# Kernel tuning notes

Measured on AMD Instinct MI355X. Metric: run time of the kernel, lower is better.

## Reference

```python
import jax, jax.numpy as jnp
import numpy as np
from jax import lax

B, C, O, H, W = 4, 96, 96, 128, 128
K = 3      # kernel size everywhere
D = 2      # dilation of dconv
KK = K * K


def conv2d(x, w, b, pad, dil=1):
    # x: [B,C,H,W], w: [O,C,K,K]
    y = lax.conv_general_dilated(
        x, w, window_strides=(1, 1), padding=[(pad, pad), (pad, pad)],
        rhs_dilation=(dil, dil), dimension_numbers=('NCHW', 'OIHW', 'NCHW'))
    return y + b[None, :, None, None]


def bilinear_sample(img, py, px):
    # img: [B,C,H,W]; py,px: [B,KK,H,W] float sample coords (zero outside)
    y0 = jnp.floor(py)
    x0 = jnp.floor(px)
    wy = py - y0
    wx = px - x0
    flat = img.reshape(B, 1, C, H * W)  # broadcast over KK

    def gather(yi, xi):
        valid = (yi >= 0) & (yi < H) & (xi >= 0) & (xi < W)
        yc = jnp.clip(yi, 0, H - 1).astype(jnp.int32)
        xc = jnp.clip(xi, 0, W - 1).astype(jnp.int32)
        idx = (yc * W + xc).reshape(B, KK, 1, H * W)
        g = jnp.take_along_axis(flat, idx, axis=3)  # [B,KK,C,H*W]
        g = g.reshape(B, KK, C, H, W)
        return g * valid.reshape(B, KK, 1, H, W)

    v00 = gather(y0, x0)
    v01 = gather(y0, x0 + 1)
    v10 = gather(y0 + 1, x0)
    v11 = gather(y0 + 1, x0 + 1)
    wy = wy[:, :, None]
    wx = wx[:, :, None]
    return ((1 - wy) * ((1 - wx) * v00 + wx * v01)
            + wy * ((1 - wx) * v10 + wx * v11))


def setup_inputs() -> dict:
    key = jax.random.key(0)
    ks = jax.random.split(key, 7)
    x = jax.random.normal(ks[0], (B, C, H, W), jnp.float32)
    s = 1.0 / np.sqrt(C * K * K)  # torch default conv init bound
    u = lambda k, shape: jax.random.uniform(k, shape, jnp.float32, -s, s)
    return dict(
        x=x,
        dconv_w=u(ks[1], (O, C, K, K)), dconv_b=u(ks[2], (O,)),
        off_w=u(ks[3], (2 * KK, C, K, K)), off_b=u(ks[4], (2 * KK,)),
        def_w=u(ks[5], (O, C, K, K)), def_b=u(ks[6], (O,)),
    )


def reference(x, dconv_w, dconv_b, off_w, off_b, def_w, def_b):
    # dilated conv + relu + residual (self.conv is unused in the original forward)
    x1 = conv2d(x, dconv_w, dconv_b, pad=D, dil=D)
    x3 = x + jax.nn.relu(x1)

    # offset prediction: [B, 2*KK, H, W] -> (dy, dx) per kernel tap
    offset = conv2d(x3, off_w, off_b, pad=1)
    off = offset.reshape(B, KK, 2, H, W)
    dy, dx = off[:, :, 0], off[:, :, 1]

    # base sampling grid: output pixel + kernel tap - padding
    ki, kj = jnp.meshgrid(jnp.arange(K), jnp.arange(K), indexing='ij')
    ky = (ki.reshape(-1) - (K - 1) // 2).astype(jnp.float32)  # [KK]
    kx = (kj.reshape(-1) - (K - 1) // 2).astype(jnp.float32)
    ygrid = jnp.arange(H, dtype=jnp.float32)[:, None]
    xgrid = jnp.arange(W, dtype=jnp.float32)[None, :]
    py = ygrid[None, None] + ky[None, :, None, None] + dy  # [B,KK,H,W]
    px = xgrid[None, None] + kx[None, :, None, None] + dx

    sampled = bilinear_sample(x3, py, px)  # [B,KK,C,H,W]
    out = jnp.einsum('bkchw,ock->bohw', sampled, def_w.reshape(O, C, KK))
    return out + def_b[None, :, None, None]
```

## Files before the change

### kernel.cpp

```cpp
#include <hip/hip_runtime.h>
#include <hip/hip_bf16.h>

#define BD 4
#define CD 96
#define OD 96
#define HD 128
#define WD 128
#define HWD (HD*WD)

typedef __attribute__((ext_vector_type(8))) short bfrag;
typedef __attribute__((ext_vector_type(4))) float ffrag;

__device__ __forceinline__ short f2bs(float f) {
    __hip_bfloat16 h = __float2bfloat16(f);
    return *reinterpret_cast<short*>(&h);
}

__device__ __forceinline__ int swizzle1024(int gid) {
    return ((gid & 7) << 7) | (gid >> 3);
}

__global__ __launch_bounds__(256) void k_transpose(const float* __restrict__ x,
                                                   short* __restrict__ xb16) {
    __shared__ short tile[128 * 104];
    int pix0 = blockIdx.x * 128;
    int b = pix0 / HWD; int hw0 = pix0 % HWD;
    int tid = threadIdx.x;

    for (int e = tid; e < 96*32; e += 256) {
        int c = e >> 5, g = e & 31;
        float4 v = *(const float4*)(x + ((size_t)(b*96 + c))*HWD + hw0 + 4*g);
        tile[(4*g+0)*104 + c] = f2bs(v.x);
        tile[(4*g+1)*104 + c] = f2bs(v.y);
        tile[(4*g+2)*104 + c] = f2bs(v.z);
        tile[(4*g+3)*104 + c] = f2bs(v.w);
    }
    __syncthreads();
    for (int e = tid; e < 128*12; e += 256) {
        int px = e / 12, c8 = e % 12;
        bfrag v = *(const bfrag*)(tile + px*104 + c8*8);
        *(bfrag*)(xb16 + ((size_t)(pix0 + px))*96 + c8*8) = v;
    }
}

__global__ void k_repack(const float* __restrict__ dconv_w,
                         const float* __restrict__ off_w,
                         const float* __restrict__ def_w,
                         short* __restrict__ wB1,
                         short* __restrict__ wB2,
                         short* __restrict__ wB) {
    int t = blockIdx.x * blockDim.x + threadIdx.x;
    if (t < 27648) {
        int j = t & 7; int l = (t >> 3) & 63; int tile = t >> 9;
        int s = tile >> 1, nt = tile & 1;
        int k = 32*s + (l >> 4)*8 + j;
        int o = 16*nt + (l & 15);
        int c = k % 96, tap = k / 96;
        wB2[t] = (o < 18) ? f2bs(off_w[(o*96 + c)*9 + tap]) : (short)0;
    }
    if (t < 82944) {
        int j = t & 7; int l = (t >> 3) & 63; int tile = t >> 9;
        int s = tile / 6, nt = tile % 6;
        int k = 32*s + (l >> 4)*8 + j;
        int o = 16*nt + (l & 15);
        int c = k % 96, tap = k / 96;
        wB1[t] = f2bs(dconv_w[(o*96 + c)*9 + tap]);
        wB[t]  = f2bs(def_w [(o*96 + c)*9 + tap]);
    }
}

__global__ __launch_bounds__(256, 4) void k_conv1(const float* __restrict__ x,
                                                  const short* __restrict__ xb16,
                                                  const short* __restrict__ wB,
                                                  const float* __restrict__ bias,
                                                  short* __restrict__ x3b) {
    int pix0 = swizzle1024(blockIdx.x) * 64;
    int b = pix0 / HWD; int hw0 = pix0 % HWD;
    int h = hw0 / WD; int w0 = hw0 % WD;
    int tid = threadIdx.x;
    int l = tid & 63, wv = tid >> 6;
    int q = l >> 4, mr = l & 15;
    int wbase = w0 + 16*wv;
    const short* xb = xb16 + ((size_t)b * HWD) * 96;
    const bfrag az = {0,0,0,0,0,0,0,0};

    ffrag acc[6];
    #pragma unroll
    for (int nt = 0; nt < 6; nt++) acc[nt] = ffrag{0.f,0.f,0.f,0.f};

    #pragma unroll 1
    for (int tap = 0; tap < 9; tap++) {
        int y = h + (tap/3)*2 - 2;
        if ((unsigned)y >= HD) continue;
        int xx = wbase + mr + (tap%3)*2 - 2;
        int xxc = min(max(xx, 0), WD-1);
        bool vx = (unsigned)xx < WD;
        const short* abase = xb + ((size_t)(y*WD + xxc))*96 + q*8;
        #pragma unroll
        for (int sc = 0; sc < 3; sc++) {
            const short* wb = wB + ((size_t)((tap*3+sc)*6)*64 + l)*8;
            bfrag a = *(const bfrag*)(abase + sc*32);
            if (!vx) a = az;
            #pragma unroll
            for (int nt = 0; nt < 6; nt++) {
                bfrag bb = *(const bfrag*)(wb + nt*512);
                acc[nt] = __builtin_amdgcn_mfma_f32_16x16x32_bf16(a, bb, acc[nt], 0, 0, 0);
            }
        }
    }

    int hwb = hw0 + 16*wv + q*4;
    #pragma unroll
    for (int nt = 0; nt < 6; nt++) {
        int o = 16*nt + mr;
        float bo = bias[o];
        float4 xr = *(const float4*)(x + ((size_t)(b*96 + o))*HWD + hwb);
        short* op = x3b + ((size_t)(b*HWD + hwb))*96 + o;
        op[0]   = f2bs(xr.x + fmaxf(acc[nt][0] + bo, 0.f));
        op[96]  = f2bs(xr.y + fmaxf(acc[nt][1] + bo, 0.f));
        op[192] = f2bs(xr.z + fmaxf(acc[nt][2] + bo, 0.f));
        op[288] = f2bs(xr.w + fmaxf(acc[nt][3] + bo, 0.f));
    }
}

__global__ __launch_bounds__(256, 4) void k_deform(const short* __restrict__ x3b,
                                                   const short* __restrict__ wB2,
                                                   const float* __restrict__ off_b,
                                                   const short* __restrict__ wB,
                                                   const float* __restrict__ def_b,
                                                   float* __restrict__ out) {
    __shared__ float offsb[64][20];

    int pix0 = swizzle1024(blockIdx.x) * 64;
    int b = pix0 / HWD; int hw0 = pix0 % HWD;
    int h = hw0 / WD; int w0 = hw0 % WD;
    int tid = threadIdx.x;
    int l = tid & 63, wv = tid >> 6;
    int q = l >> 4, mr = l & 15;
    int wbase = w0 + 16*wv;
    const short* xb = x3b + ((size_t)b * HWD) * 96;
    const bfrag az = {0,0,0,0,0,0,0,0};

    ffrag oa[2];
    oa[0] = ffrag{0.f,0.f,0.f,0.f};
    oa[1] = ffrag{0.f,0.f,0.f,0.f};

    #pragma unroll 1
    for (int tap = 0; tap < 9; tap++) {
        int y = h + tap/3 - 1;
        if ((unsigned)y >= HD) continue;
        int xx = wbase + mr + tap%3 - 1;
        int xxc = min(max(xx, 0), WD-1);
        bool vx = (unsigned)xx < WD;
        const short* abase = xb + ((size_t)(y*WD + xxc))*96 + q*8;
        #pragma unroll
        for (int sc = 0; sc < 3; sc++) {
            const short* wb = wB2 + ((size_t)((tap*3+sc)*2)*64 + l)*8;
            bfrag b0 = *(const bfrag*)(wb);
            bfrag b1 = *(const bfrag*)(wb + 512);
            bfrag a = *(const bfrag*)(abase + sc*32);
            if (!vx) a = az;
            oa[0] = __builtin_amdgcn_mfma_f32_16x16x32_bf16(a, b0, oa[0], 0, 0, 0);
            oa[1] = __builtin_amdgcn_mfma_f32_16x16x32_bf16(a, b1, oa[1], 0, 0, 0);
        }
    }
    {
        int row = 16*wv + q*4;
        float bo0 = off_b[mr];
        #pragma unroll
        for (int r = 0; r < 4; r++) offsb[row + r][mr] = oa[0][r] + bo0;
        if (mr < 2) {
            float bo1 = off_b[16 + mr];
            #pragma unroll
            for (int r = 0; r < 4; r++) offsb[row + r][16 + mr] = oa[1][r] + bo1;
        }
    }

    ffrag acc[6];
    #pragma unroll
    for (int nt = 0; nt < 6; nt++) acc[nt] = ffrag{0.f,0.f,0.f,0.f};

    #pragma unroll 1
    for (int tap = 0; tap < 9; tap++) {
        const short* pp[4];
        float fb[4];
        {
            int lp = 16*wv + mr;
            int w = wbase + mr;
            float dy = offsb[lp][2*tap];
            float dx = offsb[lp][2*tap + 1];
            float py  = (float)(h + tap/3 - 1) + dy;
            float pxf = (float)(w + tap%3 - 1) + dx;
            float y0f = floorf(py), x0f = floorf(pxf);
            float wy = py - y0f, wx = pxf - x0f;
            int y0 = (int)y0f, x0 = (int)x0f;
            int y1 = y0 + 1, x1 = x0 + 1;
            bool vy0 = (unsigned)y0 < HD, vy1 = (unsigned)y1 < HD;
            bool vx0 = (unsigned)x0 < WD, vx1 = (unsigned)x1 < WD;
            fb[0] = (vy0 && vx0) ? (1.f-wy)*(1.f-wx) : 0.f;
            fb[1] = (vy0 && vx1) ? (1.f-wy)*wx       : 0.f;
            fb[2] = (vy1 && vx0) ? wy*(1.f-wx)       : 0.f;
            fb[3] = (vy1 && vx1) ? wy*wx             : 0.f;
            int yc0 = min(max(y0,0),HD-1), yc1 = min(max(y1,0),HD-1);
            int xc0 = min(max(x0,0),WD-1), xc1 = min(max(x1,0),WD-1);
            pp[0] = xb + ((size_t)(yc0*WD + xc0))*96 + q*8;
            pp[1] = xb + ((size_t)(yc0*WD + xc1))*96 + q*8;
            pp[2] = xb + ((size_t)(yc1*WD + xc0))*96 + q*8;
            pp[3] = xb + ((size_t)(yc1*WD + xc1))*96 + q*8;
        }
        #pragma unroll
        for (int sc = 0; sc < 3; sc++) {
            int s = tap*3 + sc;
            const short* wb = wB + ((size_t)(s*6)*64 + l)*8;
            bfrag bbf[6];
            #pragma unroll
            for (int nt = 0; nt < 6; nt++) bbf[nt] = *(const bfrag*)(wb + nt*512);
            bfrag c00 = *(const bfrag*)(pp[0] + sc*32);
            bfrag c01 = *(const bfrag*)(pp[1] + sc*32);
            bfrag c10 = *(const bfrag*)(pp[2] + sc*32);
            bfrag c11 = *(const bfrag*)(pp[3] + sc*32);
            const int* i00 = (const int*)&c00;
            const int* i01 = (const int*)&c01;
            const int* i10 = (const int*)&c10;
            const int* i11 = (const int*)&c11;
            float f00 = fb[0], f01 = fb[1];
            float f10 = fb[2], f11 = fb[3];
            int ap[4];
            #pragma unroll
            for (int d = 0; d < 4; d++) {
                float a0 = __int_as_float(((unsigned)i00[d]) << 16);
                float b0f = __int_as_float(((unsigned)i01[d]) << 16);
                float c0f = __int_as_float(((unsigned)i10[d]) << 16);
                float d0 = __int_as_float(((unsigned)i11[d]) << 16);
                float a1 = __int_as_float(i00[d] & 0xffff0000);
                float b1f = __int_as_float(i01[d] & 0xffff0000);
                float c1f = __int_as_float(i10[d] & 0xffff0000);
                float d1 = __int_as_float(i11[d] & 0xffff0000);
                float rlo = f00*a0 + f01*b0f + f10*c0f + f11*d0;
                float rhi = f00*a1 + f01*b1f + f10*c1f + f11*d1;
                ap[d] = (int)((unsigned short)f2bs(rlo)) |
                        ((int)((unsigned short)f2bs(rhi)) << 16);
            }
            bfrag a = *(const bfrag*)ap;
            #pragma unroll
            for (int nt = 0; nt < 6; nt++)
                acc[nt] = __builtin_amdgcn_mfma_f32_16x16x32_bf16(a, bbf[nt], acc[nt], 0, 0, 0);
        }
    }

    int hwb = hw0 + 16*wv + q*4;
    #pragma unroll
    for (int nt = 0; nt < 6; nt++) {
        int o = 16*nt + mr;
        float bo = def_b[o];
        float4 v;
        v.x = acc[nt][0] + bo; v.y = acc[nt][1] + bo;
        v.z = acc[nt][2] + bo; v.w = acc[nt][3] + bo;
        *(float4*)(out + ((size_t)(b*96 + o))*HWD + hwb) = v;
    }
}

extern "C" void kernel_launch(void* const* d_in, const int* in_sizes, int n_in,
                              void* d_out, int out_size, void* d_ws, size_t ws_size,
                              hipStream_t stream) {
    const float* x       = (const float*)d_in[0];
    const float* dconv_w = (const float*)d_in[1];
    const float* dconv_b = (const float*)d_in[2];
    const float* off_w   = (const float*)d_in[3];
    const float* off_b   = (const float*)d_in[4];
    const float* def_w   = (const float*)d_in[5];
    const float* def_b   = (const float*)d_in[6];
    float* out = (float*)d_out;

    char* ws = (char*)d_ws;
    short* xb16 = (short*)(ws);
    short* x3b  = (short*)(ws + 12582912);
    short* wB1  = (short*)(ws + 25165824);
    short* wB2  = (short*)(ws + 25331712);
    short* wB   = (short*)(ws + 25387008);

    k_repack<<<324, 256, 0, stream>>>(dconv_w, off_w, def_w, wB1, wB2, wB);
    k_transpose<<<(BD*HWD)/128, 256, 0, stream>>>(x, xb16);
    k_conv1<<<(BD*HWD)/64, 256, 0, stream>>>(x, xb16, wB1, dconv_b, x3b);
    k_deform<<<(BD*HWD)/64, 256, 0, stream>>>(x3b, wB2, off_b, wB, def_b, out);
}
```

Baseline: 192.9 us.

## Split output channels across waves and share sampled tiles via LDS

In the conv and deformable kernels, each wave now computes two 16-pixel M tiles against half of the output channels (3 N tiles) instead of one M tile against all 6. This halves the weight fragments each wave loads and reuses each loaded weight across two A tiles. The deform kernel moves to 32-pixel, 128-thread blocks. It stages the bilinear-interpolated A fragments in a double-buffered shared buffer so both waves can use both pixel tiles, at the cost of one barrier per tap. The transpose block size is halved, launch bounds are lowered, and addressing switches to 32-bit byte offsets.

```diff
diff --git a/kernel.cpp b/kernel.cpp
--- a/kernel.cpp
+++ b/kernel.cpp
@@ -19,16 +19,19 @@
 __device__ __forceinline__ int swizzle1024(int gid) {
     return ((gid & 7) << 7) | (gid >> 3);
 }
+__device__ __forceinline__ int swizzle2048(int gid) {
+    return ((gid & 7) << 8) | (gid >> 3);
+}
 
 __global__ __launch_bounds__(256) void k_transpose(const float* __restrict__ x,
                                                    short* __restrict__ xb16) {
-    __shared__ short tile[128 * 104];
-    int pix0 = blockIdx.x * 128;
+    __shared__ short tile[64 * 104];
+    int pix0 = blockIdx.x * 64;
     int b = pix0 / HWD; int hw0 = pix0 % HWD;
     int tid = threadIdx.x;
 
-    for (int e = tid; e < 96*32; e += 256) {
-        int c = e >> 5, g = e & 31;
+    for (int e = tid; e < 96*16; e += 256) {
+        int c = e >> 4, g = e & 15;
         float4 v = *(const float4*)(x + ((size_t)(b*96 + c))*HWD + hw0 + 4*g);
         tile[(4*g+0)*104 + c] = f2bs(v.x);
         tile[(4*g+1)*104 + c] = f2bs(v.y);
@@ -36,7 +39,7 @@
         tile[(4*g+3)*104 + c] = f2bs(v.w);
     }
     __syncthreads();
-    for (int e = tid; e < 128*12; e += 256) {
+    for (int e = tid; e < 64*12; e += 256) {
         int px = e / 12, c8 = e % 12;
         bfrag v = *(const bfrag*)(tile + px*104 + c8*8);
         *(bfrag*)(xb16 + ((size_t)(pix0 + px))*96 + c8*8) = v;
@@ -69,7 +72,7 @@
     }
 }
 
-__global__ __launch_bounds__(256, 4) void k_conv1(const float* __restrict__ x,
+__global__ __launch_bounds__(256, 3) void k_conv1(const float* __restrict__ x,
                                                   const short* __restrict__ xb16,
                                                   const short* __restrict__ wB,
                                                   const float* __restrict__ bias,
@@ -79,66 +82,81 @@
     int h = hw0 / WD; int w0 = hw0 % WD;
     int tid = threadIdx.x;
     int l = tid & 63, wv = tid >> 6;
+    int pr = wv >> 1, tg = wv & 1;
     int q = l >> 4, mr = l & 15;
-    int wbase = w0 + 16*wv;
-    const short* xb = xb16 + ((size_t)b * HWD) * 96;
+    int wq = w0 + 32*pr;
+    const char* xbc = (const char*)(xb16 + ((size_t)b * HWD) * 96);
     const bfrag az = {0,0,0,0,0,0,0,0};
 
-    ffrag acc[6];
+    ffrag acc[2][3];
     #pragma unroll
-    for (int nt = 0; nt < 6; nt++) acc[nt] = ffrag{0.f,0.f,0.f,0.f};
+    for (int mt = 0; mt < 2; mt++)
+        #pragma unroll
+        for (int n = 0; n < 3; n++) acc[mt][n] = ffrag{0.f,0.f,0.f,0.f};
 
     #pragma unroll 1
     for (int tap = 0; tap < 9; tap++) {
         int y = h + (tap/3)*2 - 2;
         if ((unsigned)y >= HD) continue;
-        int xx = wbase + mr + (tap%3)*2 - 2;
-        int xxc = min(max(xx, 0), WD-1);
-        bool vx = (unsigned)xx < WD;
-        const short* abase = xb + ((size_t)(y*WD + xxc))*96 + q*8;
+        unsigned aoff[2]; bool vx[2];
+        #pragma unroll
+        for (int mt = 0; mt < 2; mt++) {
+            int xx = wq + 16*mt + mr + (tap%3)*2 - 2;
+            int xxc = min(max(xx, 0), WD-1);
+            vx[mt] = (unsigned)xx < WD;
+            aoff[mt] = (unsigned)(((y*WD + xxc)*96 + q*8) * 2);
+        }
         #pragma unroll
         for (int sc = 0; sc < 3; sc++) {
-            const short* wb = wB + ((size_t)((tap*3+sc)*6)*64 + l)*8;
-            bfrag a = *(const bfrag*)(abase + sc*32);
-            if (!vx) a = az;
-            #pragma unroll
-            for (int nt = 0; nt < 6; nt++) {
-                bfrag bb = *(const bfrag*)(wb + nt*512);
-                acc[nt] = __builtin_amdgcn_mfma_f32_16x16x32_bf16(a, bb, acc[nt], 0, 0, 0);
+            const short* wb = wB + ((size_t)((tap*3+sc)*6 + 3*tg)*64 + l)*8;
+            bfrag bb[3];
+            #pragma unroll
+            for (int n = 0; n < 3; n++) bb[n] = *(const bfrag*)(wb + n*512);
+            #pragma unroll
+            for (int mt = 0; mt < 2; mt++) {
+                bfrag a = *(const bfrag*)(xbc + aoff[mt] + sc*64);
+                if (!vx[mt]) a = az;
+                #pragma unroll
+                for (int n = 0; n < 3; n++)
+                    acc[mt][n] = __builtin_amdgcn_mfma_f32_16x16x32_bf16(a, bb[n], acc[mt][n], 0, 0, 0);
             }
         }
     }
 
-    int hwb = hw0 + 16*wv + q*4;
     #pragma unroll
-    for (int nt = 0; nt < 6; nt++) {
-        int o = 16*nt + mr;
-        float bo = bias[o];
-        float4 xr = *(const float4*)(x + ((size_t)(b*96 + o))*HWD + hwb);
-        short* op = x3b + ((size_t)(b*HWD + hwb))*96 + o;
-        op[0]   = f2bs(xr.x + fmaxf(acc[nt][0] + bo, 0.f));
-        op[96]  = f2bs(xr.y + fmaxf(acc[nt][1] + bo, 0.f));
-        op[192] = f2bs(xr.z + fmaxf(acc[nt][2] + bo, 0.f));
-        op[288] = f2bs(xr.w + fmaxf(acc[nt][3] + bo, 0.f));
-    }
-}
-
-__global__ __launch_bounds__(256, 4) void k_deform(const short* __restrict__ x3b,
+    for (int mt = 0; mt < 2; mt++) {
+        int hwb = hw0 + 32*pr + 16*mt + q*4;
+        #pragma unroll
+        for (int n = 0; n < 3; n++) {
+            int o = 16*(3*tg + n) + mr;
+            float bo = bias[o];
+            float4 xr = *(const float4*)(x + ((size_t)(b*96 + o))*HWD + hwb);
+            short* op = x3b + ((size_t)(b*HWD + hwb))*96 + o;
+            op[0]   = f2bs(xr.x + fmaxf(acc[mt][n][0] + bo, 0.f));
+            op[96]  = f2bs(xr.y + fmaxf(acc[mt][n][1] + bo, 0.f));
+            op[192] = f2bs(xr.z + fmaxf(acc[mt][n][2] + bo, 0.f));
+            op[288] = f2bs(xr.w + fmaxf(acc[mt][n][3] + bo, 0.f));
+        }
+    }
+}
+
+__global__ __launch_bounds__(128, 3) void k_deform(const short* __restrict__ x3b,
                                                    const short* __restrict__ wB2,
                                                    const float* __restrict__ off_b,
                                                    const short* __restrict__ wB,
                                                    const float* __restrict__ def_b,
                                                    float* __restrict__ out) {
-    __shared__ float offsb[64][20];
-
-    int pix0 = swizzle1024(blockIdx.x) * 64;
+    __shared__ float offsb[32][20];
+    __shared__ short abuf[2][2][3][512];
+
+    int pix0 = swizzle2048(blockIdx.x) * 32;
     int b = pix0 / HWD; int hw0 = pix0 % HWD;
     int h = hw0 / WD; int w0 = hw0 % WD;
     int tid = threadIdx.x;
-    int l = tid & 63, wv = tid >> 6;
+    int l = tid & 63, tg = tid >> 6;
     int q = l >> 4, mr = l & 15;
-    int wbase = w0 + 16*wv;
     const short* xb = x3b + ((size_t)b * HWD) * 96;
+    const char* xbc = (const char*)xb;
     const bfrag az = {0,0,0,0,0,0,0,0};
 
     ffrag oa[2];
@@ -149,23 +167,23 @@
     for (int tap = 0; tap < 9; tap++) {
         int y = h + tap/3 - 1;
         if ((unsigned)y >= HD) continue;
-        int xx = wbase + mr + tap%3 - 1;
+        int xx = w0 + 16*tg + mr + tap%3 - 1;
         int xxc = min(max(xx, 0), WD-1);
         bool vx = (unsigned)xx < WD;
-        const short* abase = xb + ((size_t)(y*WD + xxc))*96 + q*8;
+        unsigned aoff = (unsigned)(((y*WD + xxc)*96 + q*8) * 2);
         #pragma unroll
         for (int sc = 0; sc < 3; sc++) {
             const short* wb = wB2 + ((size_t)((tap*3+sc)*2)*64 + l)*8;
             bfrag b0 = *(const bfrag*)(wb);
             bfrag b1 = *(const bfrag*)(wb + 512);
-            bfrag a = *(const bfrag*)(abase + sc*32);
+            bfrag a = *(const bfrag*)(xbc + aoff + sc*64);
             if (!vx) a = az;
             oa[0] = __builtin_amdgcn_mfma_f32_16x16x32_bf16(a, b0, oa[0], 0, 0, 0);
             oa[1] = __builtin_amdgcn_mfma_f32_16x16x32_bf16(a, b1, oa[1], 0, 0, 0);
         }
     }
     {
-        int row = 16*wv + q*4;
+        int row = 16*tg + q*4;
         float bo0 = off_b[mr];
         #pragma unroll
         for (int r = 0; r < 4; r++) offsb[row + r][mr] = oa[0][r] + bo0;
@@ -176,17 +194,20 @@
         }
     }
 
-    ffrag acc[6];
+    ffrag acc[2][3];
     #pragma unroll
-    for (int nt = 0; nt < 6; nt++) acc[nt] = ffrag{0.f,0.f,0.f,0.f};
-
+    for (int mt = 0; mt < 2; mt++)
+        #pragma unroll
+        for (int n = 0; n < 3; n++) acc[mt][n] = ffrag{0.f,0.f,0.f,0.f};
+
+    int buf = 0;
     #pragma unroll 1
     for (int tap = 0; tap < 9; tap++) {
-        const short* pp[4];
+        unsigned po[4];
         float fb[4];
         {
-            int lp = 16*wv + mr;
-            int w = wbase + mr;
+            int lp = 16*tg + mr;
+            int w = w0 + lp;
             float dy = offsb[lp][2*tap];
             float dx = offsb[lp][2*tap + 1];
             float py  = (float)(h + tap/3 - 1) + dy;
@@ -203,28 +224,22 @@
             fb[3] = (vy1 && vx1) ? wy*wx             : 0.f;
             int yc0 = min(max(y0,0),HD-1), yc1 = min(max(y1,0),HD-1);
             int xc0 = min(max(x0,0),WD-1), xc1 = min(max(x1,0),WD-1);
-            pp[0] = xb + ((size_t)(yc0*WD + xc0))*96 + q*8;
-            pp[1] = xb + ((size_t)(yc0*WD + xc1))*96 + q*8;
-            pp[2] = xb + ((size_t)(yc1*WD + xc0))*96 + q*8;
-            pp[3] = xb + ((size_t)(yc1*WD + xc1))*96 + q*8;
+            po[0] = (unsigned)(((yc0*WD + xc0)*96 + q*8)*2);
+            po[1] = (unsigned)(((yc0*WD + xc1)*96 + q*8)*2);
+            po[2] = (unsigned)(((yc1*WD + xc0)*96 + q*8)*2);
+            po[3] = (unsigned)(((yc1*WD + xc1)*96 + q*8)*2);
         }
         #pragma unroll
         for (int sc = 0; sc < 3; sc++) {
-            int s = tap*3 + sc;
-            const short* wb = wB + ((size_t)(s*6)*64 + l)*8;
-            bfrag bbf[6];
-            #pragma unroll
-            for (int nt = 0; nt < 6; nt++) bbf[nt] = *(const bfrag*)(wb + nt*512);
-            bfrag c00 = *(const bfrag*)(pp[0] + sc*32);
-            bfrag c01 = *(const bfrag*)(pp[1] + sc*32);
-            bfrag c10 = *(const bfrag*)(pp[2] + sc*32);
-            bfrag c11 = *(const bfrag*)(pp[3] + sc*32);
+            bfrag c00 = *(const bfrag*)(xbc + po[0] + sc*64);
+            bfrag c01 = *(const bfrag*)(xbc + po[1] + sc*64);
+            bfrag c10 = *(const bfrag*)(xbc + po[2] + sc*64);
+            bfrag c11 = *(const bfrag*)(xbc + po[3] + sc*64);
             const int* i00 = (const int*)&c00;
             const int* i01 = (const int*)&c01;
             const int* i10 = (const int*)&c10;
             const int* i11 = (const int*)&c11;
-            float f00 = fb[0], f01 = fb[1];
-            float f10 = fb[2], f11 = fb[3];
+            float f00 = fb[0], f01 = fb[1], f10 = fb[2], f11 = fb[3];
             int ap[4];
             #pragma unroll
             for (int d = 0; d < 4; d++) {
@@ -241,22 +256,38 @@
                 ap[d] = (int)((unsigned short)f2bs(rlo)) |
                         ((int)((unsigned short)f2bs(rhi)) << 16);
             }
-            bfrag a = *(const bfrag*)ap;
-            #pragma unroll
-            for (int nt = 0; nt < 6; nt++)
-                acc[nt] = __builtin_amdgcn_mfma_f32_16x16x32_bf16(a, bbf[nt], acc[nt], 0, 0, 0);
-        }
-    }
-
-    int hwb = hw0 + 16*wv + q*4;
+            *(bfrag*)&abuf[buf][tg][sc][l*8] = *(const bfrag*)ap;
+        }
+        __syncthreads();
+        #pragma unroll
+        for (int sc = 0; sc < 3; sc++) {
+            const short* wb = wB + ((size_t)((tap*3+sc)*6 + 3*tg)*64 + l)*8;
+            bfrag bb[3];
+            #pragma unroll
+            for (int n = 0; n < 3; n++) bb[n] = *(const bfrag*)(wb + n*512);
+            bfrag a0 = *(const bfrag*)&abuf[buf][0][sc][l*8];
+            bfrag a1 = *(const bfrag*)&abuf[buf][1][sc][l*8];
+            #pragma unroll
+            for (int n = 0; n < 3; n++) {
+                acc[0][n] = __builtin_amdgcn_mfma_f32_16x16x32_bf16(a0, bb[n], acc[0][n], 0, 0, 0);
+                acc[1][n] = __builtin_amdgcn_mfma_f32_16x16x32_bf16(a1, bb[n], acc[1][n], 0, 0, 0);
+            }
+        }
+        buf ^= 1;
+    }
+
     #pragma unroll
-    for (int nt = 0; nt < 6; nt++) {
-        int o = 16*nt + mr;
-        float bo = def_b[o];
-        float4 v;
-        v.x = acc[nt][0] + bo; v.y = acc[nt][1] + bo;
-        v.z = acc[nt][2] + bo; v.w = acc[nt][3] + bo;
-        *(float4*)(out + ((size_t)(b*96 + o))*HWD + hwb) = v;
+    for (int mt = 0; mt < 2; mt++) {
+        int hwb = hw0 + 16*mt + q*4;
+        #pragma unroll
+        for (int n = 0; n < 3; n++) {
+            int o = 16*(3*tg + n) + mr;
+            float bo = def_b[o];
+            float4 v;
+            v.x = acc[mt][n][0] + bo; v.y = acc[mt][n][1] + bo;
+            v.z = acc[mt][n][2] + bo; v.w = acc[mt][n][3] + bo;
+            *(float4*)(out + ((size_t)(b*96 + o))*HWD + hwb) = v;
+        }
     }
 }
 
@@ -280,7 +311,7 @@
     short* wB   = (short*)(ws + 25387008);
 
     k_repack<<<324, 256, 0, stream>>>(dconv_w, off_w, def_w, wB1, wB2, wB);
-    k_transpose<<<(BD*HWD)/128, 256, 0, stream>>>(x, xb16);
+    k_transpose<<<(BD*HWD)/64, 256, 0, stream>>>(x, xb16);
     k_conv1<<<(BD*HWD)/64, 256, 0, stream>>>(x, xb16, wB1, dconv_b, x3b);
-    k_deform<<<(BD*HWD)/64, 256, 0, stream>>>(x3b, wB2, off_b, wB, def_b, out);
-}
+    k_deform<<<(BD*HWD)/32, 128, 0, stream>>>(x3b, wB2, off_b, wB, def_b, out);
+}
```

Measured after the change: 176.0 us. 1.1x faster.
